# Kernel optimization log

Hardware: AMD Instinct MI355X
Metric: run time of the kernel (lower is better)

## Reference

```python
import jax, jax.numpy as jnp
import numpy as np

H = 12          # n_head
DIM = 768       # model dim
HD = DIM // H   # head dim = 64
SCALE = HD ** -0.5
T = 8           # temporal frames (hardcoded in module)
N = 196         # spatial tokens (hardcoded pos-embed size)


def setup_inputs() -> dict:
    key = jax.random.key(0)
    ks = jax.random.split(key, 8)
    B = 16
    s_x = jax.random.normal(ks[0], (B * T, N + 1, DIM), dtype=jnp.float32)
    t_x = jax.random.normal(ks[1], (B, T * N, DIM), dtype=jnp.float32)
    clip_space_pos = SCALE * jax.random.normal(ks[2], (N, DIM), dtype=jnp.float32)
    vmae_space_pos = SCALE * jax.random.normal(ks[3], (N, DIM), dtype=jnp.float32)
    q_w = 0.02 * jax.random.normal(ks[4], (DIM, DIM), dtype=jnp.float32)
    q_b = jnp.zeros((DIM,), dtype=jnp.float32)
    kv_w = 0.02 * jax.random.normal(ks[5], (2 * DIM, DIM), dtype=jnp.float32)
    kv_b = jnp.zeros((2 * DIM,), dtype=jnp.float32)
    proj_w = 0.02 * jax.random.normal(ks[6], (DIM, DIM), dtype=jnp.float32)
    proj_b = jnp.zeros((DIM,), dtype=jnp.float32)
    return {"s_x": s_x, "t_x": t_x, "clip_space_pos": clip_space_pos,
            "vmae_space_pos": vmae_space_pos, "q_w": q_w, "q_b": q_b,
            "kv_w": kv_w, "kv_b": kv_b, "proj_w": proj_w, "proj_b": proj_b}


def reference(s_x, t_x, clip_space_pos, vmae_space_pos, q_w, q_b, kv_w, kv_b, proj_w, proj_b):
    B = t_x.shape[0]
    # spatial (CLIP) tokens: drop CLS, add spatial pos embed
    s_pat = s_x[:, 1:, :] + clip_space_pos            # (B*T, N, D)
    # temporal (VMAE) tokens: split frames, add spatial pos embed
    t = t_x.reshape(B * T, N, DIM) + vmae_space_pos   # (B*T, N, D)
    # q from temporal stream, kv from spatial stream (F.linear: x @ W.T + b)
    q = t @ q_w.T + q_b                               # (B*T, N, D)
    q = q.reshape(B * T, N, H, HD).transpose(0, 2, 1, 3)  # (BT, H, N, hd)
    kv = s_pat @ kv_w.T + kv_b                        # (B*T, N, 2D)
    kv = kv.reshape(B * T, N, 2, H, HD)
    k = kv[:, :, 0].transpose(0, 2, 1, 3)             # (BT, H, N, hd)
    v = kv[:, :, 1].transpose(0, 2, 1, 3)             # (BT, H, N, hd)
    attn = jnp.einsum('bhqd,bhkd->bhqk', q * SCALE, k)
    attn = jax.nn.softmax(attn, axis=-1)
    o = jnp.einsum('bhqk,bhkd->bhqd', attn, v)        # (BT, H, N, hd)
    o = o.transpose(0, 2, 1, 3).reshape(B * T, N, DIM)
    o = o @ proj_w.T + proj_b
    return o.reshape(B, T * N, DIM)
```

## Files before the change

### kernel.cpp

```cpp
#include <hip/hip_runtime.h>

typedef __bf16 bf16;
typedef __bf16 bf16x8 __attribute__((ext_vector_type(8)));
typedef __bf16 bf16x4 __attribute__((ext_vector_type(4)));
typedef float  f32x4  __attribute__((ext_vector_type(4)));
typedef float  f32x16 __attribute__((ext_vector_type(16)));
typedef unsigned int u32;

#define H_    12
#define DIM_  768
#define HD_   64
#define NTOK_ 196
#define SCALE_ 0.125f

#define GLOAD_LDS16(g, l)                                                      \
  __builtin_amdgcn_global_load_lds(                                            \
      (const __attribute__((address_space(1))) void*)(g),                      \
      (__attribute__((address_space(3))) void*)(l), 16, 0, 0)

__device__ inline u32 cvt_pk_bf16(float a, float b) {
  u32 r;
  asm volatile("v_cvt_pk_bf16_f32 %0, %1, %2" : "=v"(r) : "v"(a), "v"(b));
  return r;
}

__global__ __launch_bounds__(256) void cast_kernel(const float* __restrict__ src,
                                                   bf16* __restrict__ dst) {
  int idx = blockIdx.x * 256 + threadIdx.x;
  int e0 = idx * 8;
  const float4* s4 = (const float4*)(src + e0);
  float4 a0 = s4[0], a1 = s4[1];
  bf16x8 o;
  o[0]=(bf16)a0.x; o[1]=(bf16)a0.y; o[2]=(bf16)a0.z; o[3]=(bf16)a0.w;
  o[4]=(bf16)a1.x; o[5]=(bf16)a1.y; o[6]=(bf16)a1.z; o[7]=(bf16)a1.w;
  *(bf16x8*)(dst + e0) = o;
}

__global__ __launch_bounds__(256) void prep_kernel(const float* __restrict__ src,
                                                   const float* __restrict__ pos,
                                                   bf16* __restrict__ dst, int mode) {
  int idx = blockIdx.x * 256 + threadIdx.x;
  int e0 = idx * 8;
  int m = e0 / DIM_;
  int c = e0 - m * DIM_;
  int n = m % NTOK_;
  long srow = (mode == 0) ? (long)m : ((long)(m / NTOK_) * 197 + 1 + n);
  const float4* s4 = (const float4*)(src + srow * DIM_ + c);
  const float4* p4 = (const float4*)(pos + (long)n * DIM_ + c);
  float4 a0 = s4[0], a1 = s4[1];
  float4 b0 = p4[0], b1 = p4[1];
  bf16x8 o;
  o[0]=(bf16)(a0.x+b0.x); o[1]=(bf16)(a0.y+b0.y);
  o[2]=(bf16)(a0.z+b0.z); o[3]=(bf16)(a0.w+b0.w);
  o[4]=(bf16)(a1.x+b1.x); o[5]=(bf16)(a1.y+b1.y);
  o[6]=(bf16)(a1.z+b1.z); o[7]=(bf16)(a1.w+b1.w);
  *(bf16x8*)(dst + (long)m * DIM_ + c) = o;
}

template<int MODE, int NBX>
__global__ __launch_bounds__(256) void gemm_bt(
    const bf16* __restrict__ A, const bf16* __restrict__ Bt,
    const float* __restrict__ bias,
    bf16* __restrict__ out0, bf16* __restrict__ out1, float* __restrict__ outf) {
  __shared__ __align__(16) bf16 lds[2][2][128 * 32];
  int bm = blockIdx.x / NBX, bn = blockIdx.x % NBX;
  int tid = threadIdx.x;
  int wave = tid >> 6, lane = tid & 63;
  int g = lane >> 4, li = lane & 15;

  const bf16* Abase = A + (long)bm * 128 * 768;
  const bf16* Bbase = Bt + (long)bn * 128 * 768;

  int srow = lane >> 2;
  int sslot = lane & 3;

  auto stage = [&](int buf, int kt) {
    long kb = (long)kt * 64;
    #pragma unroll
    for (int half = 0; half < 2; ++half) {
      int c = wave + half * 4;
      int r = c * 16 + srow;
      int ss = sslot ^ ((r >> 1) & 3);
      GLOAD_LDS16((const char*)Abase + (long)r * 1536 + kb + ss * 16,
                  ((char*)&lds[buf][0][0]) + c * 1024);
      GLOAD_LDS16((const char*)Bbase + (long)r * 1536 + kb + ss * 16,
                  ((char*)&lds[buf][1][0]) + c * 1024);
    }
  };

  f32x4 acc[4][4] = {};
  int wm = wave >> 1, wn = wave & 1;
  int arow0 = wm * 64 + li, brow0 = wn * 64 + li;

  stage(0, 0);
  __syncthreads();
  int cur = 0;
  for (int kt = 0; kt < 24; ++kt) {
    if (kt < 23) stage(cur ^ 1, kt + 1);
    bf16x8 af[4], bfr[4];
    #pragma unroll
    for (int f = 0; f < 4; ++f) {
      int ra = arow0 + f * 16;
      af[f]  = *(const bf16x8*)&lds[cur][0][ra * 32 + ((g ^ ((ra >> 1) & 3)) << 3)];
      int rb = brow0 + f * 16;
      bfr[f] = *(const bf16x8*)&lds[cur][1][rb * 32 + ((g ^ ((rb >> 1) & 3)) << 3)];
    }
    #pragma unroll
    for (int mf = 0; mf < 4; ++mf)
      #pragma unroll
      for (int nf = 0; nf < 4; ++nf)
        acc[mf][nf] = __builtin_amdgcn_mfma_f32_16x16x32_bf16(af[mf], bfr[nf], acc[mf][nf], 0, 0, 0);
    __syncthreads();
    cur ^= 1;
  }

  int row_base = bm * 128 + wm * 64 + g * 4;
  int col_base = bn * 128 + wn * 64 + li;
  #pragma unroll
  for (int nf = 0; nf < 4; ++nf) {
    int col = col_base + nf * 16;
    float bv = bias[col];
    #pragma unroll
    for (int mf = 0; mf < 4; ++mf) {
      int row0 = row_base + mf * 16;
      int bt = row0 / NTOK_;
      int tok0 = row0 - bt * NTOK_;
      if (MODE == 0) {
        int hh = col >> 6, dd = col & 63;
        #pragma unroll
        for (int jj = 0; jj < 4; ++jj)
          out0[(((long)bt * H_ + hh) * NTOK_ + tok0 + jj) * HD_ + dd] =
              (bf16)((acc[mf][nf][jj] + bv) * SCALE_);
      } else if (MODE == 1) {
        if (col < DIM_) {
          int hh = col >> 6, dd = col & 63;
          #pragma unroll
          for (int jj = 0; jj < 4; ++jj)
            out0[(((long)bt * H_ + hh) * 224 + tok0 + jj) * HD_ + dd] =
                (bf16)(acc[mf][nf][jj] + bv);
        } else {
          int hh = (col - DIM_) >> 6, dd = col & 63;
          bf16x4 pk;
          #pragma unroll
          for (int jj = 0; jj < 4; ++jj) pk[jj] = (bf16)(acc[mf][nf][jj] + bv);
          *(bf16x4*)(out1 + (((long)bt * H_ + hh) * HD_ + dd) * 224 + tok0) = pk;
        }
      } else {
        #pragma unroll
        for (int jj = 0; jj < 4; ++jj)
          outf[(long)(row0 + jj) * DIM_ + col] = acc[mf][nf][jj] + bv;
      }
    }
  }
}

__global__ __launch_bounds__(448) void attn_kernel(
    const bf16* __restrict__ qws, const bf16* __restrict__ kws,
    const bf16* __restrict__ vtws, bf16* __restrict__ ows) {
  __shared__ __align__(16) bf16 k_lds[224 * 64];
  __shared__ __align__(16) bf16 vt_lds[64 * 256];
  int pair = blockIdx.x;
  int bt = pair / H_, h = pair - bt * H_;
  int tid = threadIdx.x;
  int wave = tid >> 6, lane = tid & 63;
  int hi = lane >> 5, l5 = lane & 31;

  const char* Kg = (const char*)(kws + (long)pair * 224 * 64);
  const char* Vg = (const char*)(vtws + (long)pair * 64 * 224);

  for (int ch = wave; ch < 60; ch += 7) {
    if (ch < 28) {
      int i = ch * 64 + lane;
      int r = i >> 3, p = i & 7;
      GLOAD_LDS16(Kg + (long)r * 128 + ((p ^ (r & 7)) * 16),
                  (char*)k_lds + ch * 1024);
    } else {
      int i = (ch - 28) * 64 + lane;
      int r = i >> 5, p = i & 31;
      int gs = p ^ (r & 7);
      if (gs > 27) gs = 27;
      GLOAD_LDS16(Vg + (long)r * 448 + gs * 16,
                  (char*)vt_lds + (ch - 28) * 1024);
    }
  }

  int qr = wave * 32 + l5;
  if (qr > 195) qr = 195;
  const bf16* Qp = qws + (long)pair * NTOK_ * HD_ + qr * 64 + hi * 8;
  bf16x8 qf[4];
  #pragma unroll
  for (int c = 0; c < 4; ++c) qf[c] = *(const bf16x8*)(Qp + c * 16);

  __syncthreads();

  f32x16 s[7] = {};
  #pragma unroll
  for (int kb = 0; kb < 7; ++kb) {
    #pragma unroll
    for (int c = 0; c < 4; ++c) {
      int row = kb * 32 + l5;
      bf16x8 kf = *(const bf16x8*)((char*)k_lds + row * 128 +
                                   (((c * 2 + hi) ^ (row & 7)) << 4));
      s[kb] = __builtin_amdgcn_mfma_f32_32x32x16_bf16(kf, qf[c], s[kb], 0, 0, 0);
    }
  }

  float mx = -1e30f;
  #pragma unroll
  for (int kb = 0; kb < 7; ++kb)
    #pragma unroll
    for (int reg = 0; reg < 16; ++reg) {
      int kk = kb * 32 + (reg & 3) + 8 * (reg >> 2) + 4 * hi;
      float v = s[kb][reg];
      if (kk >= NTOK_) v = -1e30f;
      s[kb][reg] = v;
      mx = fmaxf(mx, v);
    }
  mx = fmaxf(mx, __shfl_xor(mx, 32));
  float sum = 0.f;
  #pragma unroll
  for (int kb = 0; kb < 7; ++kb)
    #pragma unroll
    for (int reg = 0; reg < 16; ++reg) {
      float e = __expf(s[kb][reg] - mx);
      s[kb][reg] = e;
      sum += e;
    }
  sum += __shfl_xor(sum, 32);
  float inv = 1.f / sum;

  f32x16 o[2] = {};
  #pragma unroll
  for (int kb = 0; kb < 7; ++kb) {
    u32 w[8];
    #pragma unroll
    for (int m = 0; m < 8; ++m)
      w[m] = cvt_pk_bf16(s[kb][2 * m] * inv, s[kb][2 * m + 1] * inv);
    u32 t0 = __shfl_xor(w[0], 32), t1 = __shfl_xor(w[1], 32);
    u32 t2 = __shfl_xor(w[2], 32), t3 = __shfl_xor(w[3], 32);
    u32 u0 = __shfl_xor(w[4], 32), u1 = __shfl_xor(w[5], 32);
    u32 u2 = __shfl_xor(w[6], 32), u3 = __shfl_xor(w[7], 32);
    int4 fe = make_int4((int)(hi ? t2 : w[0]), (int)(hi ? t3 : w[1]),
                        (int)(hi ? w[2] : t0), (int)(hi ? w[3] : t1));
    int4 fo = make_int4((int)(hi ? u2 : w[4]), (int)(hi ? u3 : w[5]),
                        (int)(hi ? w[6] : u0), (int)(hi ? w[7] : u1));
    bf16x8 pe = *(bf16x8*)&fe;
    bf16x8 po = *(bf16x8*)&fo;
    #pragma unroll
    for (int dv = 0; dv < 2; ++dv) {
      int row = dv * 32 + l5;
      bf16x8 ve = *(const bf16x8*)((char*)vt_lds + row * 512 +
                                   ((((4 * kb + 0) + hi) ^ (row & 7)) << 4));
      o[dv] = __builtin_amdgcn_mfma_f32_32x32x16_bf16(pe, ve, o[dv], 0, 0, 0);
      bf16x8 vo = *(const bf16x8*)((char*)vt_lds + row * 512 +
                                   ((((4 * kb + 2) + hi) ^ (row & 7)) << 4));
      o[dv] = __builtin_amdgcn_mfma_f32_32x32x16_bf16(po, vo, o[dv], 0, 0, 0);
    }
  }

  int q_base = wave * 32;
  #pragma unroll
  for (int dv = 0; dv < 2; ++dv)
    #pragma unroll
    for (int reg = 0; reg < 16; ++reg) {
      int q = q_base + (reg & 3) + 8 * (reg >> 2) + 4 * hi;
      if (q < NTOK_)
        ows[((long)(bt * NTOK_ + q)) * DIM_ + h * HD_ + dv * 32 + l5] =
            (bf16)o[dv][reg];
    }
}

extern "C" void kernel_launch(void* const* d_in, const int* in_sizes, int n_in,
                              void* d_out, int out_size, void* d_ws, size_t ws_size,
                              hipStream_t stream) {
  const float* s_x  = (const float*)d_in[0];
  const float* t_x  = (const float*)d_in[1];
  const float* cpos = (const float*)d_in[2];
  const float* vpos = (const float*)d_in[3];
  const float* q_w  = (const float*)d_in[4];
  const float* q_b  = (const float*)d_in[5];
  const float* kv_w = (const float*)d_in[6];
  const float* kv_b = (const float*)d_in[7];
  const float* p_w  = (const float*)d_in[8];
  const float* p_b  = (const float*)d_in[9];

  char* ws = (char*)d_ws;
  const long SZ_TS = 38535168L;
  bf16* t_bf  = (bf16*)(ws);
  bf16* s_bf  = (bf16*)(ws + SZ_TS);
  bf16* wq    = (bf16*)(ws + 2 * SZ_TS);
  bf16* wkv   = (bf16*)(ws + 2 * SZ_TS + 1179648L);
  bf16* wpj   = (bf16*)(ws + 2 * SZ_TS + 3538944L);
  bf16* q_ws  = (bf16*)(ws + 2 * SZ_TS + 4718592L);
  bf16* k_ws  = (bf16*)(ws + 2 * SZ_TS + 4718592L + SZ_TS);
  bf16* vt_ws = (bf16*)(ws + 2 * SZ_TS + 4718592L + SZ_TS + 44040192L);

  cast_kernel<<<288, 256, 0, stream>>>(q_w, wq);
  cast_kernel<<<576, 256, 0, stream>>>(kv_w, wkv);
  cast_kernel<<<288, 256, 0, stream>>>(p_w, wpj);
  prep_kernel<<<9408, 256, 0, stream>>>(t_x, vpos, t_bf, 0);
  prep_kernel<<<9408, 256, 0, stream>>>(s_x, cpos, s_bf, 1);
  gemm_bt<0, 6><<<196 * 6, 256, 0, stream>>>(t_bf, wq, q_b, q_ws, nullptr, nullptr);
  gemm_bt<1, 12><<<196 * 12, 256, 0, stream>>>(s_bf, wkv, kv_b, k_ws, vt_ws, nullptr);
  attn_kernel<<<1536, 448, 0, stream>>>(q_ws, k_ws, vt_ws, t_bf);
  gemm_bt<2, 6><<<196 * 6, 256, 0, stream>>>(t_bf, wpj, p_b, nullptr, nullptr, (float*)d_out);
}
```

Before: 479.4 us.

## Merge cast and prep launches and remap GEMM workgroups across XCDs

The three weight-cast kernels become one launch, and the two activation prep kernels become one, which cuts launch count and the tail gaps between small kernels. The GEMM block index is also remapped so that consecutive logical tiles land on the same XCD (blockIdx round-robins over 8 XCDs), which is meant to improve L2 reuse of shared A/B tiles. The remap assumes 196*NBX divides evenly by 8, which holds for NBX of 6 and 12.

```diff
diff --git a/kernel.cpp b/kernel.cpp
--- a/kernel.cpp
+++ b/kernel.cpp
@@ -24,10 +24,16 @@
   return r;
 }
 
-__global__ __launch_bounds__(256) void cast_kernel(const float* __restrict__ src,
-                                                   bf16* __restrict__ dst) {
-  int idx = blockIdx.x * 256 + threadIdx.x;
-  int e0 = idx * 8;
+__global__ __launch_bounds__(256) void cast3_kernel(
+    const float* __restrict__ q_w, const float* __restrict__ kv_w,
+    const float* __restrict__ p_w, bf16* __restrict__ wq,
+    bf16* __restrict__ wkv, bf16* __restrict__ wpj) {
+  int b = blockIdx.x;
+  const float* src; bf16* dst; int base;
+  if (b < 288)      { src = q_w;  dst = wq;  base = b; }
+  else if (b < 864) { src = kv_w; dst = wkv; base = b - 288; }
+  else              { src = p_w;  dst = wpj; base = b - 864; }
+  int e0 = (base * 256 + threadIdx.x) * 8;
   const float4* s4 = (const float4*)(src + e0);
   float4 a0 = s4[0], a1 = s4[1];
   bf16x8 o;
@@ -36,10 +42,15 @@
   *(bf16x8*)(dst + e0) = o;
 }
 
-__global__ __launch_bounds__(256) void prep_kernel(const float* __restrict__ src,
-                                                   const float* __restrict__ pos,
-                                                   bf16* __restrict__ dst, int mode) {
-  int idx = blockIdx.x * 256 + threadIdx.x;
+__global__ __launch_bounds__(256) void prep2_kernel(
+    const float* __restrict__ t_x, const float* __restrict__ s_x,
+    const float* __restrict__ vpos, const float* __restrict__ cpos,
+    bf16* __restrict__ t_bf, bf16* __restrict__ s_bf) {
+  int b = blockIdx.x;
+  const float* src; const float* pos; bf16* dst; int mode;
+  if (b < 9408) { src = t_x; pos = vpos; dst = t_bf; mode = 0; }
+  else          { src = s_x; pos = cpos; dst = s_bf; mode = 1; b -= 9408; }
+  int idx = b * 256 + threadIdx.x;
   int e0 = idx * 8;
   int m = e0 / DIM_;
   int c = e0 - m * DIM_;
@@ -63,7 +74,11 @@
     const float* __restrict__ bias,
     bf16* __restrict__ out0, bf16* __restrict__ out1, float* __restrict__ outf) {
   __shared__ __align__(16) bf16 lds[2][2][128 * 32];
-  int bm = blockIdx.x / NBX, bn = blockIdx.x % NBX;
+  constexpr int NWG = 196 * NBX;
+  constexpr int CPX = NWG / 8;
+  int bid = blockIdx.x;
+  int wgid = (bid & 7) * CPX + (bid >> 3);
+  int bm = wgid / NBX, bn = wgid % NBX;
   int tid = threadIdx.x;
   int wave = tid >> 6, lane = tid & 63;
   int g = lane >> 4, li = lane & 15;
@@ -295,11 +310,8 @@
   bf16* k_ws  = (bf16*)(ws + 2 * SZ_TS + 4718592L + SZ_TS);
   bf16* vt_ws = (bf16*)(ws + 2 * SZ_TS + 4718592L + SZ_TS + 44040192L);
 
-  cast_kernel<<<288, 256, 0, stream>>>(q_w, wq);
-  cast_kernel<<<576, 256, 0, stream>>>(kv_w, wkv);
-  cast_kernel<<<288, 256, 0, stream>>>(p_w, wpj);
-  prep_kernel<<<9408, 256, 0, stream>>>(t_x, vpos, t_bf, 0);
-  prep_kernel<<<9408, 256, 0, stream>>>(s_x, cpos, s_bf, 1);
+  cast3_kernel<<<1152, 256, 0, stream>>>(q_w, kv_w, p_w, wq, wkv, wpj);
+  prep2_kernel<<<18816, 256, 0, stream>>>(t_x, s_x, vpos, cpos, t_bf, s_bf);
   gemm_bt<0, 6><<<196 * 6, 256, 0, stream>>>(t_bf, wq, q_b, q_ws, nullptr, nullptr);
   gemm_bt<1, 12><<<196 * 12, 256, 0, stream>>>(s_bf, wkv, kv_b, k_ws, vt_ws, nullptr);
   attn_kernel<<<1536, 448, 0, stream>>>(q_ws, k_ws, vt_ws, t_bf);
```

Result: faster. 454.2 us (-5.3%).
